# Kernel tuning notes

Hardware: AMD Instinct MI355X
Metric: run time of the kernel (lower is better)

## Reference

```python
import jax, jax.numpy as jnp
import numpy as np

NUM_HEADS = 4
LN_EPS = 1e-5


def layer_norm(x, g, b):
    mu = jnp.mean(x, axis=-1, keepdims=True)
    var = jnp.mean(jnp.square(x - mu), axis=-1, keepdims=True)
    return (x - mu) * jax.lax.rsqrt(var + LN_EPS) * g + b


def setup_inputs() -> dict:
    key = jax.random.key(0)
    ks = jax.random.split(key, 18)
    N, E, D = 40000, 640000, 128
    H = 4 * D  # MLP hidden
    s = 0.02
    inp = {
        'node_features': jax.random.normal(ks[0], (N, D), jnp.float32),
        'edge_index': jax.random.randint(ks[1], (2, E), 0, N, jnp.int64),
        'Wq': jax.random.normal(ks[2], (D, D), jnp.float32) * s,
        'bq': jnp.zeros((D,), jnp.float32),
        'Wk': jax.random.normal(ks[3], (D, D), jnp.float32) * s,
        'bk': jnp.zeros((D,), jnp.float32),
        'Wv': jax.random.normal(ks[4], (D, D), jnp.float32) * s,
        'bv': jnp.zeros((D,), jnp.float32),
        'Wo': jax.random.normal(ks[5], (D, D), jnp.float32) * s,
        'bo': jnp.zeros((D,), jnp.float32),
        'ln_g': jnp.ones((D,), jnp.float32),
        'ln_b': jnp.zeros((D,), jnp.float32),
        'W1': jax.random.normal(ks[6], (D, H), jnp.float32) * s,
        'b1': jnp.zeros((H,), jnp.float32),
        'W2': jax.random.normal(ks[7], (H, D), jnp.float32) * s,
        'b2': jnp.zeros((D,), jnp.float32),
    }
    return inp


def reference(node_features, edge_index, Wq, bq, Wk, bk, Wv, bv, Wo, bo,
              ln_g, ln_b, W1, b1, W2, b2):
    N, D = node_features.shape
    Hh = NUM_HEADS
    hd = D // Hh
    residual = node_features

    q = (node_features @ Wq + bq).reshape(N, Hh, hd)
    k = (node_features @ Wk + bk).reshape(N, Hh, hd)
    v = (node_features @ Wv + bv).reshape(N, Hh, hd)

    src, dst = edge_index[0], edge_index[1]
    # per-edge attention scores: [E, Hh]
    scores = jnp.einsum('ehd,ehd->eh', q[dst], k[src]) * (hd ** -0.5)

    # segment softmax over edges grouped by destination node
    seg_max = jax.ops.segment_max(scores, dst, num_segments=N)  # [N, Hh]
    seg_max = jnp.where(jnp.isfinite(seg_max), seg_max, 0.0)
    ex = jnp.exp(scores - seg_max[dst])
    seg_sum = jax.ops.segment_sum(ex, dst, num_segments=N)  # [N, Hh]
    w = ex / seg_sum[dst]  # [E, Hh]

    messages = w[:, :, None] * v[src]  # [E, Hh, hd]
    aggregated = jax.ops.segment_sum(messages, dst, num_segments=N)  # [N, Hh, hd]
    aggregated = aggregated.reshape(N, D)

    out = aggregated @ Wo + bo
    out = layer_norm(out + residual, ln_g, ln_b)
    mlp = jax.nn.gelu(out @ W1 + b1) @ W2 + b2
    return out + mlp
```

## Files before the change

### kernel.cpp

```cpp
#include <hip/hip_runtime.h>
#include <math.h>

#define D   128
#define HH  4
#define HD  32
#define HID 512
#define WPB 4
#define MT  32
#define XP  136
#define HHP 264
#define KVB 264
#define SCB 1024

typedef __attribute__((ext_vector_type(8))) short bf16x8;
typedef __attribute__((ext_vector_type(4))) float f32x4;
typedef __attribute__((ext_vector_type(2))) float f32x2;

__device__ __forceinline__ short f2b(float f) {
    unsigned u = __float_as_uint(f);
    unsigned r = (u + 0x7FFFu + ((u >> 16) & 1u)) >> 16;
    return (short)r;
}
__device__ __forceinline__ unsigned char f2fp8(float f) {
    return (unsigned char)(__builtin_amdgcn_cvt_pk_fp8_f32(f, f, 0, false) & 0xFF);
}

__device__ __forceinline__ float gelu_tanh(float x) {
    float u = 0.7978845608028654f * (x + 0.044715f * x * x * x);
    float e = __expf(2.0f * u);
    return x * e * __builtin_amdgcn_rcpf(e + 1.0f);
}

__global__ void k0_zero_deg(int* __restrict__ deg, int N) {
    int i = blockIdx.x * blockDim.x + threadIdx.x;
    if (i < N) deg[i] = 0;
}

__global__ void k_prep(const float* __restrict__ W1, const float* __restrict__ W2,
                       const float* __restrict__ Wq, const float* __restrict__ Wk,
                       const float* __restrict__ Wv, const float* __restrict__ Wo,
                       short* __restrict__ Wt1, short* __restrict__ Wt2,
                       short* __restrict__ Wtq, short* __restrict__ Wtk,
                       short* __restrict__ Wtv, short* __restrict__ Wto) {
    int i = blockIdx.x * 256 + threadIdx.x;
    {   int n = i >> 7, k = i & 127; Wt1[i] = f2b(W1[k * HID + n]); }
    {   int n = i >> 9, k = i & 511; Wt2[i] = f2b(W2[k * D + n]); }
    if (i < D * D) {
        int n = i >> 7, k = i & 127;
        Wtq[i] = f2b(Wq[k * D + n]);
        Wtk[i] = f2b(Wk[k * D + n]);
        Wtv[i] = f2b(Wv[k * D + n]);
        Wto[i] = f2b(Wo[k * D + n]);
    }
}

__global__ __launch_bounds__(256) void k1_qkv_mfma(
        const float* __restrict__ x,
        const short* __restrict__ Wtq, const float* __restrict__ bq,
        const short* __restrict__ Wtk, const float* __restrict__ bk,
        const short* __restrict__ Wtv, const float* __restrict__ bv,
        float* __restrict__ q, unsigned char* __restrict__ kv, int N) {
    __shared__ short xs[MT * XP];
    __shared__ unsigned char kvs[MT * KVB];
    int m0 = blockIdx.x * MT;
    int t = threadIdx.x;
    int wave = t >> 6, lane = t & 63, quad = lane >> 4, l16 = lane & 15;

    {
        int row = t >> 3, c0 = (t & 7) * 16;
        int n = m0 + row;
        #pragma unroll
        for (int c = 0; c < 16; c += 4) {
            float4 xv = {0.f, 0.f, 0.f, 0.f};
            if (n < N) xv = *(const float4*)(x + (size_t)n * D + c0 + c);
            xs[row * XP + c0 + c + 0] = f2b(xv.x);
            xs[row * XP + c0 + c + 1] = f2b(xv.y);
            xs[row * XP + c0 + c + 2] = f2b(xv.z);
            xs[row * XP + c0 + c + 3] = f2b(xv.w);
        }
    }
    __syncthreads();

    f32x4 accq[2][2], acck[2][2], accv[2][2];
    #pragma unroll
    for (int nt = 0; nt < 2; ++nt) {
        int c = wave * 32 + nt * 16 + l16;
        float q0 = bq[c], k0 = bk[c], v0 = bv[c];
        #pragma unroll
        for (int mt = 0; mt < 2; ++mt) {
            accq[mt][nt] = (f32x4){q0, q0, q0, q0};
            acck[mt][nt] = (f32x4){k0, k0, k0, k0};
            accv[mt][nt] = (f32x4){v0, v0, v0, v0};
        }
    }
    #pragma unroll
    for (int kt = 0; kt < 4; ++kt) {
        int klane = kt * 32 + quad * 8;
        bf16x8 a0 = *(const bf16x8*)(xs + (l16)      * XP + klane);
        bf16x8 a1 = *(const bf16x8*)(xs + (16 + l16) * XP + klane);
        #pragma unroll
        for (int nt = 0; nt < 2; ++nt) {
            int c = wave * 32 + nt * 16 + l16;
            bf16x8 fq = *(const bf16x8*)(Wtq + (size_t)c * D + klane);
            bf16x8 fk = *(const bf16x8*)(Wtk + (size_t)c * D + klane);
            bf16x8 fv = *(const bf16x8*)(Wtv + (size_t)c * D + klane);
            accq[0][nt] = __builtin_amdgcn_mfma_f32_16x16x32_bf16(a0, fq, accq[0][nt], 0, 0, 0);
            accq[1][nt] = __builtin_amdgcn_mfma_f32_16x16x32_bf16(a1, fq, accq[1][nt], 0, 0, 0);
            acck[0][nt] = __builtin_amdgcn_mfma_f32_16x16x32_bf16(a0, fk, acck[0][nt], 0, 0, 0);
            acck[1][nt] = __builtin_amdgcn_mfma_f32_16x16x32_bf16(a1, fk, acck[1][nt], 0, 0, 0);
            accv[0][nt] = __builtin_amdgcn_mfma_f32_16x16x32_bf16(a0, fv, accv[0][nt], 0, 0, 0);
            accv[1][nt] = __builtin_amdgcn_mfma_f32_16x16x32_bf16(a1, fv, accv[1][nt], 0, 0, 0);
        }
    }
    #pragma unroll
    for (int mt = 0; mt < 2; ++mt)
        #pragma unroll
        for (int nt = 0; nt < 2; ++nt)
            #pragma unroll
            for (int r = 0; r < 4; ++r) {
                int row = mt * 16 + quad * 4 + r;
                int n = m0 + row;
                int c = wave * 32 + nt * 16 + l16;
                if (n < N) q[(size_t)n * D + c] = accq[mt][nt][r];
                int base = row * KVB + 16 * (c >> 3) + (c & 7);
                kvs[base]     = f2fp8(acck[mt][nt][r]);
                kvs[base + 8] = f2fp8(accv[mt][nt][r]);
            }
    __syncthreads();
    {
        int row = t >> 3, c0 = (t & 7) * 32;
        int n = m0 + row;
        if (n < N) {
            *(uint4*)(kv + (size_t)n * 256 + c0) =
                *(const uint4*)(kvs + row * KVB + c0);
            *(uint4*)(kv + (size_t)n * 256 + c0 + 16) =
                *(const uint4*)(kvs + row * KVB + c0 + 16);
        }
    }
}

__global__ void k_hist(const int* __restrict__ dst, int* __restrict__ deg, int E) {
    int i = blockIdx.x * blockDim.x + threadIdx.x;
    if (i < E) atomicAdd(&deg[dst[i]], 1);
}

__global__ void k_scan1(const int* __restrict__ deg, int* __restrict__ partial, int N) {
    __shared__ int red[256];
    int b = blockIdx.x, t = threadIdx.x;
    int base = b * SCB + t * 4;
    int s = 0;
    #pragma unroll
    for (int i = 0; i < 4; ++i) { int idx = base + i; if (idx < N) s += deg[idx]; }
    red[t] = s;
    __syncthreads();
    for (int off = 128; off > 0; off >>= 1) {
        if (t < off) red[t] += red[t + off];
        __syncthreads();
    }
    if (t == 0) partial[b] = red[0];
}

__global__ void k_scan2(int* __restrict__ partial, int nb) {
    __shared__ int s[256];
    int t = threadIdx.x;
    int v0 = (t < nb) ? partial[t] : 0;
    s[t] = v0;
    __syncthreads();
    for (int off = 1; off < 256; off <<= 1) {
        int v = (t >= off) ? s[t - off] : 0;
        __syncthreads();
        s[t] += v;
        __syncthreads();
    }
    if (t < nb) partial[t] = s[t] - v0;
    if (t == nb - 1) partial[nb] = s[t];
}

__global__ void k_scan3(const int* __restrict__ deg, const int* __restrict__ partial,
                        int* __restrict__ row_ptr, int* __restrict__ cursor,
                        int N, int nb) {
    __shared__ int red[256];
    int b = blockIdx.x, t = threadIdx.x;
    int base = b * SCB + t * 4;
    int d0[4]; int s = 0;
    #pragma unroll
    for (int i = 0; i < 4; ++i) {
        int idx = base + i;
        d0[i] = (idx < N) ? deg[idx] : 0;
        s += d0[i];
    }
    red[t] = s;
    __syncthreads();
    for (int off = 1; off < 256; off <<= 1) {
        int v = (t >= off) ? red[t - off] : 0;
        __syncthreads();
        red[t] += v;
        __syncthreads();
    }
    int off0 = partial[b] + red[t] - s;
    #pragma unroll
    for (int i = 0; i < 4; ++i) {
        int idx = base + i;
        if (idx < N) { row_ptr[idx] = off0; cursor[idx] = off0; off0 += d0[i]; }
    }
    if (b == 0 && t == 0) row_ptr[N] = partial[nb];
}

__global__ void k_scatter(const int* __restrict__ src, const int* __restrict__ dst,
                          int* __restrict__ cursor, int* __restrict__ col, int E) {
    int i = blockIdx.x * blockDim.x + threadIdx.x;
    if (i < E) {
        int d = dst[i];
        int pos = atomicAdd(&cursor[d], 1);
        col[pos] = src[i];
    }
}

__global__ void k_attn(const float* __restrict__ q, const unsigned char* __restrict__ kv,
                       const int* __restrict__ row_ptr, const int* __restrict__ col,
                       float* __restrict__ agg, int N) {
    int wave = threadIdx.x >> 6;
    int lane = threadIdx.x & 63;
    int g = lane >> 4, s = lane & 15;
    int n = blockIdx.x * WPB + wave;
    if (n >= N) return;
    int beg = row_ptr[n], end = row_ptr[n + 1];

    float4 qa = *(const float4*)(q + (size_t)n * D + 8 * s);
    float4 qb = *(const float4*)(q + (size_t)n * D + 8 * s + 4);

    float acc[8] = {0.f, 0.f, 0.f, 0.f, 0.f, 0.f, 0.f, 0.f};
    float l = 0.f;

    int np = (end - beg + 3) >> 2;
    uint4 pk_cur = {0, 0, 0, 0};
    int idx_next = 0;
    if (np > 0) {
        int c0 = col[min(beg + g, end - 1)];
        pk_cur = *(const uint4*)(kv + (size_t)c0 * 256 + 16 * s);
        if (np > 1) idx_next = col[min(beg + 4 + g, end - 1)];
    }
    for (int it = 0; it < np; ++it) {
        uint4 pk = pk_cur;
        bool valid = (beg + it * 4 + g) < end;
        if (it + 1 < np) {
            pk_cur = *(const uint4*)(kv + (size_t)idx_next * 256 + 16 * s);
            if (it + 2 < np)
                idx_next = col[min(beg + (it + 2) * 4 + g, end - 1)];
        }
        f32x2 k01 = __builtin_amdgcn_cvt_pk_f32_fp8((int)pk.x, false);
        f32x2 k23 = __builtin_amdgcn_cvt_pk_f32_fp8((int)pk.x, true);
        f32x2 k45 = __builtin_amdgcn_cvt_pk_f32_fp8((int)pk.y, false);
        f32x2 k67 = __builtin_amdgcn_cvt_pk_f32_fp8((int)pk.y, true);
        f32x2 v01 = __builtin_amdgcn_cvt_pk_f32_fp8((int)pk.z, false);
        f32x2 v23 = __builtin_amdgcn_cvt_pk_f32_fp8((int)pk.z, true);
        f32x2 v45 = __builtin_amdgcn_cvt_pk_f32_fp8((int)pk.w, false);
        f32x2 v67 = __builtin_amdgcn_cvt_pk_f32_fp8((int)pk.w, true);
        float d = qa.x * k01.x + qa.y * k01.y + qa.z * k23.x + qa.w * k23.y
                + qb.x * k45.x + qb.y * k45.y + qb.z * k67.x + qb.w * k67.y;
        d += __shfl_xor(d, 1);
        d += __shfl_xor(d, 2);
        float pe = __expf(d * 0.17677669529663687f);
        pe = valid ? pe : 0.f;
        l += pe;
        acc[0] = fmaf(pe, v01.x, acc[0]);
        acc[1] = fmaf(pe, v01.y, acc[1]);
        acc[2] = fmaf(pe, v23.x, acc[2]);
        acc[3] = fmaf(pe, v23.y, acc[3]);
        acc[4] = fmaf(pe, v45.x, acc[4]);
        acc[5] = fmaf(pe, v45.y, acc[5]);
        acc[6] = fmaf(pe, v67.x, acc[6]);
        acc[7] = fmaf(pe, v67.y, acc[7]);
    }
    #pragma unroll
    for (int m = 16; m <= 32; m <<= 1) {
        l += __shfl_xor(l, m);
        #pragma unroll
        for (int i = 0; i < 8; ++i) acc[i] += __shfl_xor(acc[i], m);
    }
    if (g == 0) {
        float inv = (l > 0.f) ? 1.f / l : 0.f;
        float4 o1 = {acc[0] * inv, acc[1] * inv, acc[2] * inv, acc[3] * inv};
        float4 o2 = {acc[4] * inv, acc[5] * inv, acc[6] * inv, acc[7] * inv};
        *(float4*)(agg + (size_t)n * D + 8 * s)     = o1;
        *(float4*)(agg + (size_t)n * D + 8 * s + 4) = o2;
    }
}

__global__ __launch_bounds__(256) void k56_wo_ln_mlp(
        const float* __restrict__ agg, const short* __restrict__ Wto,
        const float* __restrict__ bo, const float* __restrict__ x,
        const float* __restrict__ g, const float* __restrict__ b,
        const short* __restrict__ Wt1, const float* __restrict__ b1,
        const short* __restrict__ Wt2, const float* __restrict__ b2,
        float* __restrict__ out, int N) {
    __shared__ short xs[MT * XP];
    __shared__ short hid[MT * HHP];
    __shared__ float ps[MT * 4], ps2[MT * 4];
    int m0 = blockIdx.x * MT;
    int t = threadIdx.x;
    int wave = t >> 6, lane = t & 63, quad = lane >> 4, l16 = lane & 15;

    {
        int row = t >> 3, c0 = (t & 7) * 16;
        int n = m0 + row;
        #pragma unroll
        for (int c = 0; c < 16; c += 4) {
            float4 xv = {0.f, 0.f, 0.f, 0.f};
            if (n < N) xv = *(const float4*)(agg + (size_t)n * D + c0 + c);
            xs[row * XP + c0 + c + 0] = f2b(xv.x);
            xs[row * XP + c0 + c + 1] = f2b(xv.y);
            xs[row * XP + c0 + c + 2] = f2b(xv.z);
            xs[row * XP + c0 + c + 3] = f2b(xv.w);
        }
    }
    __syncthreads();

    f32x4 acc[2][2];
    #pragma unroll
    for (int nt = 0; nt < 2; ++nt) {
        float bb = bo[wave * 32 + nt * 16 + l16];
        acc[0][nt] = (f32x4){bb, bb, bb, bb};
        acc[1][nt] = (f32x4){bb, bb, bb, bb};
    }
    #pragma unroll
    for (int kt = 0; kt < 4; ++kt) {
        int klane = kt * 32 + quad * 8;
        bf16x8 a0 = *(const bf16x8*)(xs + (l16)      * XP + klane);
        bf16x8 a1 = *(const bf16x8*)(xs + (16 + l16) * XP + klane);
        #pragma unroll
        for (int nt = 0; nt < 2; ++nt) {
            bf16x8 bf = *(const bf16x8*)(Wto + (size_t)(wave * 32 + nt * 16 + l16) * D + klane);
            acc[0][nt] = __builtin_amdgcn_mfma_f32_16x16x32_bf16(a0, bf, acc[0][nt], 0, 0, 0);
            acc[1][nt] = __builtin_amdgcn_mfma_f32_16x16x32_bf16(a1, bf, acc[1][nt], 0, 0, 0);
        }
    }
    float lnval[2][2][4];
    #pragma unroll
    for (int mt = 0; mt < 2; ++mt)
        #pragma unroll
        for (int nt = 0; nt < 2; ++nt)
            #pragma unroll
            for (int r = 0; r < 4; ++r) {
                int n = m0 + mt * 16 + quad * 4 + r;
                int c = wave * 32 + nt * 16 + l16;
                float v = acc[mt][nt][r];
                if (n < N) v += x[(size_t)n * D + c];
                lnval[mt][nt][r] = v;
            }

    #pragma unroll
    for (int mt = 0; mt < 2; ++mt)
        #pragma unroll
        for (int r = 0; r < 4; ++r) {
            float a0 = lnval[mt][0][r], a1 = lnval[mt][1][r];
            float s1 = a0 + a1;
            float s2 = a0 * a0 + a1 * a1;
            #pragma unroll
            for (int m = 1; m <= 8; m <<= 1) {
                s1 += __shfl_xor(s1, m);
                s2 += __shfl_xor(s2, m);
            }
            if (l16 == 0) {
                int row = mt * 16 + quad * 4 + r;
                ps[row * 4 + wave] = s1;
                ps2[row * 4 + wave] = s2;
            }
        }
    __syncthreads();

    #pragma unroll
    for (int mt = 0; mt < 2; ++mt)
        #pragma unroll
        for (int r = 0; r < 4; ++r) {
            int row = mt * 16 + quad * 4 + r;
            float4 p1 = *(const float4*)(ps + row * 4);
            float4 p2 = *(const float4*)(ps2 + row * 4);
            float mm = (p1.x + p1.y + p1.z + p1.w) * (1.0f / D);
            float m2 = (p2.x + p2.y + p2.z + p2.w) * (1.0f / D);
            float rs = rsqrtf(m2 - mm * mm + 1e-5f);
            #pragma unroll
            for (int nt = 0; nt < 2; ++nt) {
                int c = wave * 32 + nt * 16 + l16;
                float v = (lnval[mt][nt][r] - mm) * rs * g[c] + b[c];
                lnval[mt][nt][r] = v;
                xs[row * XP + c] = f2b(v);
            }
        }
    __syncthreads();

    f32x4 acc2[2][2];
    #pragma unroll
    for (int nt = 0; nt < 2; ++nt) {
        float bb = b2[wave * 32 + nt * 16 + l16];
        acc2[0][nt] = (f32x4){bb, bb, bb, bb};
        acc2[1][nt] = (f32x4){bb, bb, bb, bb};
    }
    #pragma unroll
    for (int h = 0; h < 2; ++h) {
        f32x4 acc1[2][4];
        #pragma unroll
        for (int nt = 0; nt < 4; ++nt) {
            float bb = b1[h * 256 + wave * 64 + nt * 16 + l16];
            acc1[0][nt] = (f32x4){bb, bb, bb, bb};
            acc1[1][nt] = (f32x4){bb, bb, bb, bb};
        }
        #pragma unroll
        for (int kt = 0; kt < 4; ++kt) {
            int klane = kt * 32 + quad * 8;
            bf16x8 a0 = *(const bf16x8*)(xs + (l16)      * XP + klane);
            bf16x8 a1 = *(const bf16x8*)(xs + (16 + l16) * XP + klane);
            #pragma unroll
            for (int nt = 0; nt < 4; ++nt) {
                int hc = h * 256 + wave * 64 + nt * 16 + l16;
                bf16x8 bf = *(const bf16x8*)(Wt1 + (size_t)hc * D + klane);
                acc1[0][nt] = __builtin_amdgcn_mfma_f32_16x16x32_bf16(a0, bf, acc1[0][nt], 0, 0, 0);
                acc1[1][nt] = __builtin_amdgcn_mfma_f32_16x16x32_bf16(a1, bf, acc1[1][nt], 0, 0, 0);
            }
        }
        __syncthreads();
        #pragma unroll
        for (int mt = 0; mt < 2; ++mt)
            #pragma unroll
            for (int nt = 0; nt < 4; ++nt)
                #pragma unroll
                for (int r = 0; r < 4; ++r) {
                    int row = mt * 16 + quad * 4 + r;
                    int lc = wave * 64 + nt * 16 + l16;
                    hid[row * HHP + lc] = f2b(gelu_tanh(acc1[mt][nt][r]));
                }
        __syncthreads();
        #pragma unroll
        for (int kt = 0; kt < 8; ++kt) {
            int klane = kt * 32 + quad * 8;
            bf16x8 a0 = *(const bf16x8*)(hid + (l16)      * HHP + klane);
            bf16x8 a1 = *(const bf16x8*)(hid + (16 + l16) * HHP + klane);
            #pragma unroll
            for (int nt = 0; nt < 2; ++nt) {
                bf16x8 bf = *(const bf16x8*)(Wt2 + (size_t)(wave * 32 + nt * 16 + l16) * HID
                                             + h * 256 + klane);
                acc2[0][nt] = __builtin_amdgcn_mfma_f32_16x16x32_bf16(a0, bf, acc2[0][nt], 0, 0, 0);
                acc2[1][nt] = __builtin_amdgcn_mfma_f32_16x16x32_bf16(a1, bf, acc2[1][nt], 0, 0, 0);
            }
        }
    }

    #pragma unroll
    for (int mt = 0; mt < 2; ++mt)
        #pragma unroll
        for (int nt = 0; nt < 2; ++nt)
            #pragma unroll
            for (int r = 0; r < 4; ++r) {
                int n = m0 + mt * 16 + quad * 4 + r;
                int c = wave * 32 + nt * 16 + l16;
                if (n < N)
                    out[(size_t)n * D + c] = lnval[mt][nt][r] + acc2[mt][nt][r];
            }
}

extern "C" void kernel_launch(void* const* d_in, const int* in_sizes, int n_in,
                              void* d_out, int out_size, void* d_ws, size_t ws_size,
                              hipStream_t stream) {
    const float* x   = (const float*)d_in[0];
    const int*   ei  = (const int*)d_in[1];
    const float* Wq  = (const float*)d_in[2];
    const float* bq  = (const float*)d_in[3];
    const float* Wk  = (const float*)d_in[4];
    const float* bk  = (const float*)d_in[5];
    const float* Wv  = (const float*)d_in[6];
    const float* bv  = (const float*)d_in[7];
    const float* Wo  = (const float*)d_in[8];
    const float* bo  = (const float*)d_in[9];
    const float* lng = (const float*)d_in[10];
    const float* lnb = (const float*)d_in[11];
    const float* W1  = (const float*)d_in[12];
    const float* b1  = (const float*)d_in[13];
    const float* W2  = (const float*)d_in[14];
    const float* b2  = (const float*)d_in[15];
    float* out = (float*)d_out;

    int N = in_sizes[0] / D;
    int E = in_sizes[1] / 2;
    const int* srcp = ei;
    const int* dstp = ei + E;

    short* Wt1 = (short*)d_ws;
    short* Wt2 = Wt1 + 512 * 128;
    short* Wtq = Wt2 + 512 * 128;
    short* Wtk = Wtq + 128 * 128;
    short* Wtv = Wtk + 128 * 128;
    short* Wto = Wtv + 128 * 128;
    float* q   = (float*)(Wto + 128 * 128);
    unsigned char* kv = (unsigned char*)(q + (size_t)N * D);
    float* agg = (float*)(kv + (size_t)N * 256);
    int*   deg     = (int*)(agg + (size_t)N * D);
    int*   row_ptr = deg + N;
    int*   cursor  = row_ptr + N + 1;
    int*   col     = cursor + N;
    int*   partial = col + E;

    int nblk32 = (N + MT - 1) / MT;
    int eblk   = (E + 255) / 256;
    int nbs    = (N + SCB - 1) / SCB;

    k0_zero_deg<<<(N + 255) / 256, 256, 0, stream>>>(deg, N);
    k_prep<<<(512 * 128) / 256, 256, 0, stream>>>(W1, W2, Wq, Wk, Wv, Wo,
                                                  Wt1, Wt2, Wtq, Wtk, Wtv, Wto);
    k_hist<<<eblk, 256, 0, stream>>>(dstp, deg, E);
    k1_qkv_mfma<<<nblk32, 256, 0, stream>>>(x, Wtq, bq, Wtk, bk, Wtv, bv, q, kv, N);
    k_scan1<<<nbs, 256, 0, stream>>>(deg, partial, N);
    k_scan2<<<1, 256, 0, stream>>>(partial, nbs);
    k_scan3<<<nbs, 256, 0, stream>>>(deg, partial, row_ptr, cursor, N, nbs);
    k_scatter<<<eblk, 256, 0, stream>>>(srcp, dstp, cursor, col, E);
    k_attn<<<(N + WPB - 1) / WPB, WPB * 64, 0, stream>>>(q, kv, row_ptr, col, agg, N);
    k56_wo_ln_mlp<<<nblk32, 256, 0, stream>>>(agg, Wto, bo, x, lng, lnb,
                                              Wt1, b1, Wt2, b2, out, N);
}
```

Baseline: 277.4 us.

## Store attention output as bf16 and give each wave its own 16-row tile

The attention kernel now writes its aggregated output in bf16 instead of fp32, halving that intermediate's write and read traffic. The fused Wo/LayerNorm/MLP kernel is restructured so each wave owns a 16-row tile and computes all 128 output columns. The LayerNorm reduction therefore stays inside a wave, every __syncthreads disappears, and the A operand comes straight from global memory. The trade-offs are that each wave reloads every weight tile itself, register pressure rises with 8 accumulators per GEMM, and the residual path now uses the bf16-rounded LayerNorm output, which costs some precision.

Result: slower. 342.8 us (+23.6%).

```diff
diff --git a/kernel.cpp b/kernel.cpp
--- a/kernel.cpp
+++ b/kernel.cpp
@@ -8,7 +8,6 @@
 #define WPB 4
 #define MT  32
 #define XP  136
-#define HHP 264
 #define KVB 264
 #define SCB 1024
 
@@ -20,6 +19,9 @@
     unsigned u = __float_as_uint(f);
     unsigned r = (u + 0x7FFFu + ((u >> 16) & 1u)) >> 16;
     return (short)r;
+}
+__device__ __forceinline__ float b2f(short s) {
+    return __uint_as_float(((unsigned)(unsigned short)s) << 16);
 }
 __device__ __forceinline__ unsigned char f2fp8(float f) {
     return (unsigned char)(__builtin_amdgcn_cvt_pk_fp8_f32(f, f, 0, false) & 0xFF);
@@ -218,7 +220,7 @@
 
 __global__ void k_attn(const float* __restrict__ q, const unsigned char* __restrict__ kv,
                        const int* __restrict__ row_ptr, const int* __restrict__ col,
-                       float* __restrict__ agg, int N) {
+                       short* __restrict__ aggb, int N) {
     int wave = threadIdx.x >> 6;
     int lane = threadIdx.x & 63;
     int g = lane >> 4, s = lane & 15;
@@ -280,182 +282,135 @@
     }
     if (g == 0) {
         float inv = (l > 0.f) ? 1.f / l : 0.f;
-        float4 o1 = {acc[0] * inv, acc[1] * inv, acc[2] * inv, acc[3] * inv};
-        float4 o2 = {acc[4] * inv, acc[5] * inv, acc[6] * inv, acc[7] * inv};
-        *(float4*)(agg + (size_t)n * D + 8 * s)     = o1;
-        *(float4*)(agg + (size_t)n * D + 8 * s + 4) = o2;
+        bf16x8 o;
+        #pragma unroll
+        for (int i = 0; i < 8; ++i) o[i] = f2b(acc[i] * inv);
+        *(bf16x8*)(aggb + (size_t)n * D + 8 * s) = o;
     }
 }
 
 __global__ __launch_bounds__(256) void k56_wo_ln_mlp(
-        const float* __restrict__ agg, const short* __restrict__ Wto,
+        const short* __restrict__ aggb, const short* __restrict__ Wto,
         const float* __restrict__ bo, const float* __restrict__ x,
         const float* __restrict__ g, const float* __restrict__ b,
         const short* __restrict__ Wt1, const float* __restrict__ b1,
         const short* __restrict__ Wt2, const float* __restrict__ b2,
         float* __restrict__ out, int N) {
-    __shared__ short xs[MT * XP];
-    __shared__ short hid[MT * HHP];
-    __shared__ float ps[MT * 4], ps2[MT * 4];
-    int m0 = blockIdx.x * MT;
+    __shared__ short lns[4 * 16 * XP];
+    __shared__ short hids[4 * 16 * XP];
     int t = threadIdx.x;
     int wave = t >> 6, lane = t & 63, quad = lane >> 4, l16 = lane & 15;
-
-    {
-        int row = t >> 3, c0 = (t & 7) * 16;
-        int n = m0 + row;
-        #pragma unroll
-        for (int c = 0; c < 16; c += 4) {
-            float4 xv = {0.f, 0.f, 0.f, 0.f};
-            if (n < N) xv = *(const float4*)(agg + (size_t)n * D + c0 + c);
-            xs[row * XP + c0 + c + 0] = f2b(xv.x);
-            xs[row * XP + c0 + c + 1] = f2b(xv.y);
-            xs[row * XP + c0 + c + 2] = f2b(xv.z);
-            xs[row * XP + c0 + c + 3] = f2b(xv.w);
-        }
-    }
-    __syncthreads();
-
-    f32x4 acc[2][2];
-    #pragma unroll
-    for (int nt = 0; nt < 2; ++nt) {
-        float bb = bo[wave * 32 + nt * 16 + l16];
-        acc[0][nt] = (f32x4){bb, bb, bb, bb};
-        acc[1][nt] = (f32x4){bb, bb, bb, bb};
-    }
+    int base = blockIdx.x * 64 + wave * 16;
+    short* lnt  = lns  + wave * 16 * XP;
+    short* hidt = hids + wave * 16 * XP;
+
+    f32x4 acc[8];
+    #pragma unroll
+    for (int nt = 0; nt < 8; ++nt) {
+        float bb = bo[nt * 16 + l16];
+        acc[nt] = (f32x4){bb, bb, bb, bb};
+    }
+    int arow = min(base + l16, N - 1);
     #pragma unroll
     for (int kt = 0; kt < 4; ++kt) {
-        int klane = kt * 32 + quad * 8;
-        bf16x8 a0 = *(const bf16x8*)(xs + (l16)      * XP + klane);
-        bf16x8 a1 = *(const bf16x8*)(xs + (16 + l16) * XP + klane);
-        #pragma unroll
-        for (int nt = 0; nt < 2; ++nt) {
-            bf16x8 bf = *(const bf16x8*)(Wto + (size_t)(wave * 32 + nt * 16 + l16) * D + klane);
-            acc[0][nt] = __builtin_amdgcn_mfma_f32_16x16x32_bf16(a0, bf, acc[0][nt], 0, 0, 0);
-            acc[1][nt] = __builtin_amdgcn_mfma_f32_16x16x32_bf16(a1, bf, acc[1][nt], 0, 0, 0);
-        }
-    }
-    float lnval[2][2][4];
-    #pragma unroll
-    for (int mt = 0; mt < 2; ++mt)
-        #pragma unroll
-        for (int nt = 0; nt < 2; ++nt)
+        bf16x8 a = *(const bf16x8*)(aggb + (size_t)arow * D + kt * 32 + quad * 8);
+        #pragma unroll
+        for (int nt = 0; nt < 8; ++nt) {
+            bf16x8 bf = *(const bf16x8*)(Wto + (size_t)(nt * 16 + l16) * D + kt * 32 + quad * 8);
+            acc[nt] = __builtin_amdgcn_mfma_f32_16x16x32_bf16(a, bf, acc[nt], 0, 0, 0);
+        }
+    }
+    float lnv[8][4];
+    #pragma unroll
+    for (int r = 0; r < 4; ++r) {
+        int nr = min(base + quad * 4 + r, N - 1);
+        #pragma unroll
+        for (int nt = 0; nt < 8; ++nt)
+            lnv[nt][r] = acc[nt][r] + x[(size_t)nr * D + nt * 16 + l16];
+    }
+    #pragma unroll
+    for (int r = 0; r < 4; ++r) {
+        float s1 = 0.f, s2 = 0.f;
+        #pragma unroll
+        for (int nt = 0; nt < 8; ++nt) {
+            float v = lnv[nt][r];
+            s1 += v; s2 += v * v;
+        }
+        #pragma unroll
+        for (int m = 1; m <= 8; m <<= 1) {
+            s1 += __shfl_xor(s1, m);
+            s2 += __shfl_xor(s2, m);
+        }
+        float mm = s1 * (1.0f / D), m2 = s2 * (1.0f / D);
+        float rs = rsqrtf(m2 - mm * mm + 1e-5f);
+        int row = quad * 4 + r;
+        #pragma unroll
+        for (int nt = 0; nt < 8; ++nt) {
+            int c = nt * 16 + l16;
+            float v = (lnv[nt][r] - mm) * rs * g[c] + b[c];
+            lnt[row * XP + c] = f2b(v);
+        }
+    }
+
+    f32x4 acc2[8];
+    #pragma unroll
+    for (int nt = 0; nt < 8; ++nt) {
+        float bb = b2[nt * 16 + l16];
+        acc2[nt] = (f32x4){bb, bb, bb, bb};
+    }
+    bf16x8 la[4];
+    #pragma unroll
+    for (int kt = 0; kt < 4; ++kt)
+        la[kt] = *(const bf16x8*)(lnt + l16 * XP + kt * 32 + quad * 8);
+
+    #pragma unroll
+    for (int h = 0; h < 4; ++h) {
+        f32x4 acc1[8];
+        #pragma unroll
+        for (int j = 0; j < 8; ++j) {
+            float bb = b1[h * 128 + j * 16 + l16];
+            acc1[j] = (f32x4){bb, bb, bb, bb};
+        }
+        #pragma unroll
+        for (int kt = 0; kt < 4; ++kt) {
+            #pragma unroll
+            for (int j = 0; j < 8; ++j) {
+                bf16x8 bf = *(const bf16x8*)(Wt1 + (size_t)(h * 128 + j * 16 + l16) * D
+                                             + kt * 32 + quad * 8);
+                acc1[j] = __builtin_amdgcn_mfma_f32_16x16x32_bf16(la[kt], bf, acc1[j], 0, 0, 0);
+            }
+        }
+        #pragma unroll
+        for (int j = 0; j < 8; ++j)
             #pragma unroll
             for (int r = 0; r < 4; ++r) {
-                int n = m0 + mt * 16 + quad * 4 + r;
-                int c = wave * 32 + nt * 16 + l16;
-                float v = acc[mt][nt][r];
-                if (n < N) v += x[(size_t)n * D + c];
-                lnval[mt][nt][r] = v;
+                int row = quad * 4 + r;
+                hidt[row * XP + j * 16 + l16] = f2b(gelu_tanh(acc1[j][r]));
             }
-
-    #pragma unroll
-    for (int mt = 0; mt < 2; ++mt)
-        #pragma unroll
-        for (int r = 0; r < 4; ++r) {
-            float a0 = lnval[mt][0][r], a1 = lnval[mt][1][r];
-            float s1 = a0 + a1;
-            float s2 = a0 * a0 + a1 * a1;
+        #pragma unroll
+        for (int kt = 0; kt < 4; ++kt) {
+            bf16x8 ha = *(const bf16x8*)(hidt + l16 * XP + kt * 32 + quad * 8);
             #pragma unroll
-            for (int m = 1; m <= 8; m <<= 1) {
-                s1 += __shfl_xor(s1, m);
-                s2 += __shfl_xor(s2, m);
+            for (int nt = 0; nt < 8; ++nt) {
+                bf16x8 bf = *(const bf16x8*)(Wt2 + (size_t)(nt * 16 + l16) * HID
+                                             + h * 128 + kt * 32 + quad * 8);
+                acc2[nt] = __builtin_amdgcn_mfma_f32_16x16x32_bf16(ha, bf, acc2[nt], 0, 0, 0);
             }
-            if (l16 == 0) {
-                int row = mt * 16 + quad * 4 + r;
-                ps[row * 4 + wave] = s1;
-                ps2[row * 4 + wave] = s2;
+        }
+    }
+
+    #pragma unroll
+    for (int r = 0; r < 4; ++r) {
+        int row = quad * 4 + r;
+        int n = base + row;
+        if (n < N) {
+            #pragma unroll
+            for (int nt = 0; nt < 8; ++nt) {
+                int c = nt * 16 + l16;
+                out[(size_t)n * D + c] = b2f(lnt[row * XP + c]) + acc2[nt][r];
             }
         }
-    __syncthreads();
-
-    #pragma unroll
-    for (int mt = 0; mt < 2; ++mt)
-        #pragma unroll
-        for (int r = 0; r < 4; ++r) {
-            int row = mt * 16 + quad * 4 + r;
-            float4 p1 = *(const float4*)(ps + row * 4);
-            float4 p2 = *(const float4*)(ps2 + row * 4);
-            float mm = (p1.x + p1.y + p1.z + p1.w) * (1.0f / D);
-            float m2 = (p2.x + p2.y + p2.z + p2.w) * (1.0f / D);
-            float rs = rsqrtf(m2 - mm * mm + 1e-5f);
-            #pragma unroll
-            for (int nt = 0; nt < 2; ++nt) {
-                int c = wave * 32 + nt * 16 + l16;
-                float v = (lnval[mt][nt][r] - mm) * rs * g[c] + b[c];
-                lnval[mt][nt][r] = v;
-                xs[row * XP + c] = f2b(v);
-            }
-        }
-    __syncthreads();
-
-    f32x4 acc2[2][2];
-    #pragma unroll
-    for (int nt = 0; nt < 2; ++nt) {
-        float bb = b2[wave * 32 + nt * 16 + l16];
-        acc2[0][nt] = (f32x4){bb, bb, bb, bb};
-        acc2[1][nt] = (f32x4){bb, bb, bb, bb};
-    }
-    #pragma unroll
-    for (int h = 0; h < 2; ++h) {
-        f32x4 acc1[2][4];
-        #pragma unroll
-        for (int nt = 0; nt < 4; ++nt) {
-            float bb = b1[h * 256 + wave * 64 + nt * 16 + l16];
-            acc1[0][nt] = (f32x4){bb, bb, bb, bb};
-            acc1[1][nt] = (f32x4){bb, bb, bb, bb};
-        }
-        #pragma unroll
-        for (int kt = 0; kt < 4; ++kt) {
-            int klane = kt * 32 + quad * 8;
-            bf16x8 a0 = *(const bf16x8*)(xs + (l16)      * XP + klane);
-            bf16x8 a1 = *(const bf16x8*)(xs + (16 + l16) * XP + klane);
-            #pragma unroll
-            for (int nt = 0; nt < 4; ++nt) {
-                int hc = h * 256 + wave * 64 + nt * 16 + l16;
-                bf16x8 bf = *(const bf16x8*)(Wt1 + (size_t)hc * D + klane);
-                acc1[0][nt] = __builtin_amdgcn_mfma_f32_16x16x32_bf16(a0, bf, acc1[0][nt], 0, 0, 0);
-                acc1[1][nt] = __builtin_amdgcn_mfma_f32_16x16x32_bf16(a1, bf, acc1[1][nt], 0, 0, 0);
-            }
-        }
-        __syncthreads();
-        #pragma unroll
-        for (int mt = 0; mt < 2; ++mt)
-            #pragma unroll
-            for (int nt = 0; nt < 4; ++nt)
-                #pragma unroll
-                for (int r = 0; r < 4; ++r) {
-                    int row = mt * 16 + quad * 4 + r;
-                    int lc = wave * 64 + nt * 16 + l16;
-                    hid[row * HHP + lc] = f2b(gelu_tanh(acc1[mt][nt][r]));
-                }
-        __syncthreads();
-        #pragma unroll
-        for (int kt = 0; kt < 8; ++kt) {
-            int klane = kt * 32 + quad * 8;
-            bf16x8 a0 = *(const bf16x8*)(hid + (l16)      * HHP + klane);
-            bf16x8 a1 = *(const bf16x8*)(hid + (16 + l16) * HHP + klane);
-            #pragma unroll
-            for (int nt = 0; nt < 2; ++nt) {
-                bf16x8 bf = *(const bf16x8*)(Wt2 + (size_t)(wave * 32 + nt * 16 + l16) * HID
-                                             + h * 256 + klane);
-                acc2[0][nt] = __builtin_amdgcn_mfma_f32_16x16x32_bf16(a0, bf, acc2[0][nt], 0, 0, 0);
-                acc2[1][nt] = __builtin_amdgcn_mfma_f32_16x16x32_bf16(a1, bf, acc2[1][nt], 0, 0, 0);
-            }
-        }
-    }
-
-    #pragma unroll
-    for (int mt = 0; mt < 2; ++mt)
-        #pragma unroll
-        for (int nt = 0; nt < 2; ++nt)
-            #pragma unroll
-            for (int r = 0; r < 4; ++r) {
-                int n = m0 + mt * 16 + quad * 4 + r;
-                int c = wave * 32 + nt * 16 + l16;
-                if (n < N)
-                    out[(size_t)n * D + c] = lnval[mt][nt][r] + acc2[mt][nt][r];
-            }
+    }
 }
 
 extern "C" void kernel_launch(void* const* d_in, const int* in_sizes, int n_in,
@@ -492,14 +447,15 @@
     short* Wto = Wtv + 128 * 128;
     float* q   = (float*)(Wto + 128 * 128);
     unsigned char* kv = (unsigned char*)(q + (size_t)N * D);
-    float* agg = (float*)(kv + (size_t)N * 256);
-    int*   deg     = (int*)(agg + (size_t)N * D);
+    short* aggb = (short*)(kv + (size_t)N * 256);
+    int*   deg     = (int*)(aggb + (size_t)N * D);
     int*   row_ptr = deg + N;
     int*   cursor  = row_ptr + N + 1;
     int*   col     = cursor + N;
     int*   partial = col + E;
 
     int nblk32 = (N + MT - 1) / MT;
+    int nblk64 = (N + 63) / 64;
     int eblk   = (E + 255) / 256;
     int nbs    = (N + SCB - 1) / SCB;
 
@@ -512,7 +468,7 @@
     k_scan2<<<1, 256, 0, stream>>>(partial, nbs);
     k_scan3<<<nbs, 256, 0, stream>>>(deg, partial, row_ptr, cursor, N, nbs);
     k_scatter<<<eblk, 256, 0, stream>>>(srcp, dstp, cursor, col, E);
-    k_attn<<<(N + WPB - 1) / WPB, WPB * 64, 0, stream>>>(q, kv, row_ptr, col, agg, N);
-    k56_wo_ln_mlp<<<nblk32, 256, 0, stream>>>(agg, Wto, bo, x, lng, lnb,
+    k_attn<<<(N + WPB - 1) / WPB, WPB * 64, 0, stream>>>(q, kv, row_ptr, col, aggb, N);
+    k56_wo_ln_mlp<<<nblk64, 256, 0, stream>>>(aggb, Wto, bo, x, lng, lnb,
                                               Wt1, b1, Wt2, b2, out, N);
 }
```
